# Kernel optimization log

Measured on AMD Instinct MI355X. Metric: run time of the kernel, lower is better.

## Reference

```python
import jax, jax.numpy as jnp
import numpy as np

EPS = 1e-5
# NOTE: TransmorpherLayer2d passes (dim_head, num_heads) into TiedAxialSelfAttention2d(num_heads, dim_head),
# so with init dim_head=64, num_heads=8 the attention effectively uses H=64 heads of C=8 channels each.
H = 64
C = 8


def _ln_ch(x, w, b):
    # AxialLayerNorm over channel dim (dim=1) of [B, D, S, L]
    m = x.mean(axis=1, keepdims=True)
    v = x.var(axis=1, keepdims=True)
    return (x - m) * jax.lax.rsqrt(v + EPS) * w[None, :, None, None] + b[None, :, None, None]


def _conv1x1(x, W, b):
    # Conv2d kernel_size=1: pointwise channel mix. W: [out, in], x: [B, in, S, L]
    return jnp.einsum('od,bdsl->bosl', W, x) + b[None, :, None, None]


def setup_inputs() -> dict:
    key = jax.random.key(0)
    ks = jax.random.split(key, 8)
    B, D, S, L, F = 1, 512, 64, 256, 2048
    g = lambda k, shape: jax.random.normal(k, shape, jnp.float32) * 0.02
    return {
        'x': jax.random.normal(ks[0], (B, D, S, L), jnp.float32),
        'w_row': g(ks[1], (3 * D, D)), 'b_row': jnp.zeros((3 * D,), jnp.float32),
        'w_col': g(ks[2], (3 * D, D)), 'b_col': jnp.zeros((3 * D,), jnp.float32),
        'w_an1': jnp.ones((D,), jnp.float32), 'b_an1': jnp.zeros((D,), jnp.float32),
        'w_an2': jnp.ones((D,), jnp.float32), 'b_an2': jnp.zeros((D,), jnp.float32),
        'w_ff1': g(ks[3], (F, D)), 'b_ff1': jnp.zeros((F,), jnp.float32),
        'w_ff2': g(ks[4], (D, F)), 'b_ff2': jnp.zeros((D,), jnp.float32),
        'w_ln1': jnp.ones((D,), jnp.float32), 'b_ln1': jnp.zeros((D,), jnp.float32),
        'w_ln2': jnp.ones((D,), jnp.float32), 'b_ln2': jnp.zeros((D,), jnp.float32),
    }


def _forward(x, w_row, b_row, w_col, b_col, w_an1, b_an1, w_an2, b_an2,
             w_ff1, b_ff1, w_ff2, b_ff2, w_ln1, b_ln1, w_ln2, b_ln2):
    B, D, S, L = x.shape
    # ---- tied row attention (attention tied across the S axis; no 1/sqrt scaling in source) ----
    qkv = _conv1x1(x, w_row, b_row)
    q, k, v = [t.reshape(B, H, C, S, L) for t in jnp.split(qkv, 3, axis=1)]
    row_attn = jax.nn.softmax(jnp.einsum('bhcsi,bhcsj->bhij', q, k), axis=-1)  # [B,H,L,L]
    row_out = jnp.einsum('bhij,bhdsj->bhdsi', row_attn, v).reshape(B, D, S, L)
    out = _ln_ch(x + row_out, w_an1, b_an1)
    # ---- column attention (softmax over key index j = dim -2) ----
    qkv = _conv1x1(out, w_col, b_col)
    q, k, v = [t.reshape(B, H, C, S, L) for t in jnp.split(qkv, 3, axis=1)]
    col_attn = jax.nn.softmax(jnp.einsum('bhcil,bhcjl->bhijl', q, k), axis=-2)  # [B,H,S,S,L]
    col_out = jnp.einsum('bhijl,bhdjl->bhdil', col_attn, v).reshape(B, D, S, L)
    attn_out = _ln_ch(out + col_out, w_an2, b_an2)
    # ---- layer body. Source bug kept faithfully: the attention residual `x + dropout1(out)`
    # is computed then discarded; norm1 is applied to the attention output only. ----
    h = _ln_ch(attn_out, w_ln1, b_ln1)
    ff = _conv1x1(jax.nn.relu(_conv1x1(h, w_ff1, b_ff1)), w_ff2, b_ff2)
    return _ln_ch(h + ff, w_ln2, b_ln2)


def reference(x, w_row, b_row, w_col, b_col, w_an1, b_an1, w_an2, b_an2,
              w_ff1, b_ff1, w_ff2, b_ff2, w_ln1, b_ln1, w_ln2, b_ln2):
    return _forward(x, w_row, b_row, w_col, b_col, w_an1, b_an1, w_an2, b_an2,
                    w_ff1, b_ff1, w_ff2, b_ff2, w_ln1, b_ln1, w_ln2, b_ln2)
```

## Files before the change

### kernel.cpp

```cpp
#include <hip/hip_runtime.h>
#include <hip/hip_bf16.h>

using s16x8 = __attribute__((ext_vector_type(8))) short;
using f32x4 = __attribute__((ext_vector_type(4))) float;
using u32x2 = __attribute__((ext_vector_type(2))) unsigned;

__device__ __forceinline__ ushort f2bf(float f) {
  union { float f; unsigned u; } v; v.f = f;
  unsigned r = v.u + 0x7fffu + ((v.u >> 16) & 1u);
  return (ushort)(r >> 16);
}
__device__ __forceinline__ float bf2f(ushort u) {
  return __uint_as_float(((unsigned)u) << 16);
}
__device__ __forceinline__ void gload16(const void* g, void* l) {
  __builtin_amdgcn_global_load_lds(
      (const __attribute__((address_space(1))) void*)g,
      (__attribute__((address_space(3))) void*)l, 16, 0, 0);
}

template<int AF, int BF, bool BIAS, bool RELU, int OUT, bool TRC>
__global__ __launch_bounds__(256)
void gemm(void* __restrict__ Cv, const ushort* __restrict__ A,
          const ushort* __restrict__ B, const float* __restrict__ bias,
          int K, int lda, int ldb, int ldc, long sA, long sB, long sC)
{
  __shared__ ushort As[2][5120];
  __shared__ ushort Bs[2][5120];
  const int tid  = threadIdx.x;
  const int lane = tid & 63, wid = tid >> 6;
  const int m0 = blockIdx.y * 128, n0 = blockIdx.x * 128;
  A += (long)blockIdx.z * sA;
  B += (long)blockIdx.z * sB;

  const int wm = (wid >> 1) * 64, wn = (wid & 1) * 64;
  const int fr = lane & 15, kg = lane >> 4;

  f32x4 acc[4][4];
#pragma unroll
  for (int i = 0; i < 4; ++i)
#pragma unroll
    for (int j = 0; j < 4; ++j)
#pragma unroll
      for (int r = 0; r < 4; ++r) acc[i][j][r] = 0.f;

  auto stageT = [&](const ushort* __restrict__ G, int ld, int c0,
                    ushort* lds, int k0) {
#pragma unroll
    for (int c = 0; c < 2; ++c) {
      const int nb = wid * 2 + c;
      const ushort* gp = G + (long)(k0 + (lane >> 1)) * ld + c0 + nb * 16 + (lane & 1) * 8;
      gload16(gp, lds + nb * 512);
    }
  };
  auto loadN = [&](const ushort* __restrict__ G, int ld, int r0, int k0,
                   uint4& x, uint4& y) {
    const ushort* gp = G + (long)(r0 + (tid >> 1)) * ld + k0 + (tid & 1) * 8;
    x = *(const uint4*)gp;
    y = *(const uint4*)(gp + 16);
  };
  auto writeN = [&](ushort* lds, uint4 x, uint4 y) {
    ushort* p = lds + (tid >> 1) * 40 + (tid & 1) * 8;
    *(uint4*)p = x;
    *(uint4*)(p + 16) = y;
  };
  auto fragN = [&](const ushort* lds, int row) {
    union { s16x8 f; u32x2 h[2]; } u;
    const ushort* p = lds + row * 40 + kg * 4;
    u.h[0] = *(const u32x2*)p;
    u.h[1] = *(const u32x2*)(p + 16);
    return u.f;
  };
  auto fragT = [&](const ushort* lds, int rb) {
    union { s16x8 f; u32x2 h[2]; } u;
    unsigned base = (unsigned)(unsigned long long)(lds + rb * 512) + lane * 8;
    asm volatile("ds_read_b64_tr_b16 %0, %1" : "=v"(u.h[0]) : "v"(base));
    asm volatile("ds_read_b64_tr_b16 %0, %1 offset:512" : "=v"(u.h[1]) : "v"(base));
    return u.f;
  };

  const int NT = K >> 5;
  uint4 ax, ay, bx, by;

  if constexpr (AF == 0) { loadN(A, lda, m0, 0, ax, ay); writeN(As[0], ax, ay); }
  else                   { stageT(A, lda, m0, As[0], 0); }
  if constexpr (BF == 0) { loadN(B, ldb, n0, 0, bx, by); writeN(Bs[0], bx, by); }
  else                   { stageT(B, ldb, n0, Bs[0], 0); }
  __syncthreads();

  for (int t = 0; t < NT; ++t) {
    const int cur = t & 1, nxt = cur ^ 1;
    const bool pre = (t + 1) < NT;
    if (pre) {
      if constexpr (AF == 0) loadN(A, lda, m0, (t + 1) << 5, ax, ay);
      else                   stageT(A, lda, m0, As[nxt], (t + 1) << 5);
      if constexpr (BF == 0) loadN(B, ldb, n0, (t + 1) << 5, bx, by);
      else                   stageT(B, ldb, n0, Bs[nxt], (t + 1) << 5);
    }
    s16x8 af[4], bv[4];
#pragma unroll
    for (int m = 0; m < 4; ++m) {
      if constexpr (AF == 0) af[m] = fragN(As[cur], wm + m * 16 + fr);
      else                   af[m] = fragT(As[cur], (wm >> 4) + m);
    }
#pragma unroll
    for (int n = 0; n < 4; ++n) {
      if constexpr (BF == 0) bv[n] = fragN(Bs[cur], wn + n * 16 + fr);
      else                   bv[n] = fragT(Bs[cur], (wn >> 4) + n);
    }
    if constexpr (AF == 1 || BF == 1) {
      asm volatile("s_waitcnt lgkmcnt(0)");
      __builtin_amdgcn_sched_barrier(0);
    }
    __builtin_amdgcn_s_setprio(1);
#pragma unroll
    for (int m = 0; m < 4; ++m)
#pragma unroll
      for (int n = 0; n < 4; ++n)
        acc[m][n] = __builtin_amdgcn_mfma_f32_16x16x32_bf16(af[m], bv[n], acc[m][n], 0, 0, 0);
    __builtin_amdgcn_s_setprio(0);
    if (pre) {
      if constexpr (AF == 0) writeN(As[nxt], ax, ay);
      if constexpr (BF == 0) writeN(Bs[nxt], bx, by);
    }
    __syncthreads();
  }

#pragma unroll
  for (int m = 0; m < 4; ++m) {
    const int rowb = m0 + wm + m * 16 + kg * 4;
#pragma unroll
    for (int n = 0; n < 4; ++n) {
      const int col = n0 + wn + n * 16 + fr;
      f32x4 v = acc[m][n];
      if constexpr (BIAS) {
#pragma unroll
        for (int r = 0; r < 4; ++r) v[r] += bias[rowb + r];
      }
      if constexpr (RELU) {
#pragma unroll
        for (int r = 0; r < 4; ++r) v[r] = fmaxf(v[r], 0.f);
      }
      if constexpr (TRC) {
        float* C = (float*)Cv + (long)blockIdx.z * sC;
        float4 s; s.x = v[0]; s.y = v[1]; s.z = v[2]; s.w = v[3];
        *(float4*)(C + (long)col * ldc + rowb) = s;
      } else if constexpr (OUT == 0) {
        float* C = (float*)Cv + (long)blockIdx.z * sC;
#pragma unroll
        for (int r = 0; r < 4; ++r) C[(long)(rowb + r) * ldc + col] = v[r];
      } else {
        ushort* C = (ushort*)Cv + (long)blockIdx.z * sC;
#pragma unroll
        for (int r = 0; r < 4; ++r) C[(long)(rowb + r) * ldc + col] = f2bf(v[r]);
      }
    }
  }
}

__global__ __launch_bounds__(256)
void cvt_kernel(const float4* __restrict__ in, ushort4* __restrict__ out, int n4) {
  int i = blockIdx.x * 256 + threadIdx.x;
  if (i < n4) {
    float4 f = in[i];
    ushort4 u; u.x = f2bf(f.x); u.y = f2bf(f.y); u.z = f2bf(f.z); u.w = f2bf(f.w);
    out[i] = u;
  }
}

__global__ __launch_bounds__(256)
void softmax_kernel(const float* __restrict__ S, ushort* __restrict__ P) {
  const int row = blockIdx.x * 4 + (threadIdx.x >> 6);
  const int lane = threadIdx.x & 63;
  float4 v = *(const float4*)(S + (long)row * 256 + lane * 4);
  float mx = fmaxf(fmaxf(v.x, v.y), fmaxf(v.z, v.w));
#pragma unroll
  for (int off = 32; off; off >>= 1) mx = fmaxf(mx, __shfl_xor(mx, off));
  v.x = __expf(v.x - mx); v.y = __expf(v.y - mx);
  v.z = __expf(v.z - mx); v.w = __expf(v.w - mx);
  float s = v.x + v.y + v.z + v.w;
#pragma unroll
  for (int off = 32; off; off >>= 1) s += __shfl_xor(s, off);
  const float r = 1.f / s;
  ushort4 o;
  o.x = f2bf(v.x * r); o.y = f2bf(v.y * r); o.z = f2bf(v.z * r); o.w = f2bf(v.w * r);
  *(ushort4*)(P + (long)row * 256 + lane * 4) = o;
}

__global__ __launch_bounds__(256)
void colattn_kernel(const ushort* __restrict__ qkv, float* __restrict__ out) {
  __shared__ float q[4][8][64], kk[4][8][64], vv[4][8][64];
  const int h = blockIdx.y;
  const int l0 = blockIdx.x * 4;
  const int tid = threadIdx.x;
  for (int i = tid; i < 1536; i += 256) {
    int m = i >> 9;
    int e = i & 511;
    int c = e >> 6, s = e & 63;
    ushort4 u = *(const ushort4*)(qkv + (long)(m * 512 + h * 8 + c) * 16384 + s * 256 + l0);
    float* dst = (m == 0) ? &q[0][0][0] : (m == 1) ? &kk[0][0][0] : &vv[0][0][0];
    dst[e] = bf2f(u.x); dst[512 + e] = bf2f(u.y);
    dst[1024 + e] = bf2f(u.z); dst[1536 + e] = bf2f(u.w);
  }
  __syncthreads();
  const int li = tid >> 6, lane = tid & 63;
  float qi[8];
#pragma unroll
  for (int c = 0; c < 8; ++c) qi[c] = q[li][c][lane];
  float sc[64];
#pragma unroll
  for (int j = 0; j < 64; ++j) {
    float s = 0.f;
#pragma unroll
    for (int c = 0; c < 8; ++c) s += qi[c] * kk[li][c][j];
    sc[j] = s;
  }
  float mx = sc[0];
#pragma unroll
  for (int j = 1; j < 64; ++j) mx = fmaxf(mx, sc[j]);
  float sum = 0.f;
#pragma unroll
  for (int j = 0; j < 64; ++j) { sc[j] = __expf(sc[j] - mx); sum += sc[j]; }
  const float rs = 1.f / sum;
  float o[8];
#pragma unroll
  for (int c = 0; c < 8; ++c) o[c] = 0.f;
#pragma unroll
  for (int j = 0; j < 64; ++j)
#pragma unroll
    for (int c = 0; c < 8; ++c) o[c] += sc[j] * vv[li][c][j];
#pragma unroll
  for (int c = 0; c < 8; ++c) q[li][c][lane] = o[c] * rs;
  __syncthreads();
  for (int i = tid; i < 512; i += 256) {
    int c = i >> 6, s = i & 63;
    float4 f; f.x = q[0][c][s]; f.y = q[1][c][s]; f.z = q[2][c][s]; f.w = q[3][c][s];
    *(float4*)(out + (long)(h * 8 + c) * 16384 + s * 256 + l0) = f;
  }
}

template<bool RES, bool BFO>
__global__ __launch_bounds__(256)
void ln_kernel(float* __restrict__ out, ushort* __restrict__ bfo,
               const float* __restrict__ a, const float* __restrict__ b,
               const float* __restrict__ w, const float* __restrict__ bias) {
  __shared__ float red[8][64];
  const int lane = threadIdx.x & 63;
  const int seg = threadIdx.x >> 6;
  const long n = (long)blockIdx.x * 64 + lane;
  float s1 = 0.f, s2 = 0.f;
  for (int d = seg * 128; d < seg * 128 + 128; ++d) {
    float v = a[(long)d * 16384 + n];
    if constexpr (RES) v += b[(long)d * 16384 + n];
    s1 += v; s2 += v * v;
  }
  red[seg][lane] = s1; red[4 + seg][lane] = s2;
  __syncthreads();
  s1 = red[0][lane] + red[1][lane] + red[2][lane] + red[3][lane];
  s2 = red[4][lane] + red[5][lane] + red[6][lane] + red[7][lane];
  const float mean = s1 * (1.f / 512.f);
  const float var = s2 * (1.f / 512.f) - mean * mean;
  const float rstd = rsqrtf(var + 1e-5f);
  for (int d = seg * 128; d < seg * 128 + 128; ++d) {
    float v = a[(long)d * 16384 + n];
    if constexpr (RES) v += b[(long)d * 16384 + n];
    float o = (v - mean) * rstd * w[d] + bias[d];
    out[(long)d * 16384 + n] = o;
    if constexpr (BFO) bfo[(long)d * 16384 + n] = f2bf(o);
  }
}

extern "C" void kernel_launch(void* const* d_in, const int* in_sizes, int n_in,
                              void* d_out, int out_size, void* d_ws, size_t ws_size,
                              hipStream_t stream) {
  const float* x     = (const float*)d_in[0];
  const float* w_row = (const float*)d_in[1];
  const float* b_row = (const float*)d_in[2];
  const float* w_col = (const float*)d_in[3];
  const float* b_col = (const float*)d_in[4];
  const float* w_an1 = (const float*)d_in[5];
  const float* b_an1 = (const float*)d_in[6];
  const float* w_an2 = (const float*)d_in[7];
  const float* b_an2 = (const float*)d_in[8];
  const float* w_ff1 = (const float*)d_in[9];
  const float* b_ff1 = (const float*)d_in[10];
  const float* w_ff2 = (const float*)d_in[11];
  const float* b_ff2 = (const float*)d_in[12];
  const float* w_ln1 = (const float*)d_in[13];
  const float* b_ln1 = (const float*)d_in[14];
  const float* w_ln2 = (const float*)d_in[15];
  const float* b_ln2 = (const float*)d_in[16];
  float* outp = (float*)d_out;

  char* Wb = (char*)d_ws;
  ushort* big   = (ushort*)Wb;
  float*  sc    = (float*)(Wb + (size_t)1536 * 16384 * 2);
  float*  bufA  = (float*)(Wb + 67108864ull);
  float*  bufB  = (float*)(Wb + 100663296ull);
  float*  bufC  = (float*)(Wb + 134217728ull);
  ushort* P     = (ushort*)bufC;
  ushort* actbf = (ushort*)(Wb + 167772160ull);
  ushort* xbf   = actbf;
  ushort* wrowb = (ushort*)(Wb + 184549376ull);
  ushort* wcolb = wrowb + 786432;
  ushort* wff1b = wcolb + 786432;
  ushort* wff2b = wff1b + 1048576;

  const dim3 blk(256);
  const long HQ = 131072;
  const long HS = 65536;

  cvt_kernel<<<8192, blk, 0, stream>>>((const float4*)x, (ushort4*)xbf, 2097152);
  cvt_kernel<<<768,  blk, 0, stream>>>((const float4*)w_row, (ushort4*)wrowb, 196608);
  cvt_kernel<<<768,  blk, 0, stream>>>((const float4*)w_col, (ushort4*)wcolb, 196608);
  cvt_kernel<<<1024, blk, 0, stream>>>((const float4*)w_ff1, (ushort4*)wff1b, 262144);
  cvt_kernel<<<1024, blk, 0, stream>>>((const float4*)w_ff2, (ushort4*)wff2b, 262144);

  gemm<0,1,true,false,1,false><<<dim3(128, 12, 1), blk, 0, stream>>>(
      big, wrowb, xbf, b_row, 512, 512, 16384, 16384, 0, 0, 0);
  gemm<1,1,false,false,0,false><<<dim3(2, 2, 64), blk, 0, stream>>>(
      sc, big, big + (long)512 * 16384, nullptr, 512, 256, 256, 256, HQ, HQ, HS);
  softmax_kernel<<<4096, blk, 0, stream>>>(sc, P);
  gemm<0,0,false,false,0,true><<<dim3(4, 2, 64), blk, 0, stream>>>(
      bufA, P, big + (long)1024 * 16384, nullptr, 256, 256, 256, 256, HS, HQ, HQ);
  ln_kernel<true, true><<<256, blk, 0, stream>>>(bufB, actbf, x, bufA, w_an1, b_an1);
  gemm<0,1,true,false,1,false><<<dim3(128, 12, 1), blk, 0, stream>>>(
      big, wcolb, actbf, b_col, 512, 512, 16384, 16384, 0, 0, 0);
  colattn_kernel<<<dim3(64, 64), blk, 0, stream>>>(big, bufA);
  ln_kernel<true, false><<<256, blk, 0, stream>>>(bufC, nullptr, bufB, bufA, w_an2, b_an2);
  ln_kernel<false, true><<<256, blk, 0, stream>>>(bufB, actbf, bufC, nullptr, w_ln1, b_ln1);
  gemm<0,1,true,true,1,false><<<dim3(128, 16, 1), blk, 0, stream>>>(
      big, wff1b, actbf, b_ff1, 512, 512, 16384, 16384, 0, 0, 0);
  gemm<0,1,true,false,0,false><<<dim3(128, 4, 1), blk, 0, stream>>>(
      bufA, wff2b, big, b_ff2, 2048, 2048, 16384, 16384, 0, 0, 0);
  ln_kernel<true, false><<<256, blk, 0, stream>>>(outp, nullptr, bufB, bufA, w_ln2, b_ln2);
}
```

Baseline: 531.1 us.

## Swizzle block order for XCD locality, fuse back-to-back layernorms, cache LN values in registers

GEMM and column-attention blocks are remapped so that consecutive workgroups, which round-robin across XCDs, cover contiguous tiles, aiming at better L2 reuse. Layernorm kernels now use 1024 threads and keep each element in registers, so the input is read once instead of twice. The two consecutive layernorms after column attention are fused into one kernel with two reductions, dropping an intermediate fp32 buffer round trip. The fused kernel reads from and writes to bufB in place, which is safe only because every element is held in registers before any write.

```diff
diff --git a/kernel.cpp b/kernel.cpp
--- a/kernel.cpp
+++ b/kernel.cpp
@@ -29,7 +29,10 @@
   __shared__ ushort Bs[2][5120];
   const int tid  = threadIdx.x;
   const int lane = tid & 63, wid = tid >> 6;
-  const int m0 = blockIdx.y * 128, n0 = blockIdx.x * 128;
+  const int nwg = gridDim.x * gridDim.y;
+  const int lin = blockIdx.y * gridDim.x + blockIdx.x;
+  const int swz = ((nwg & 7) == 0) ? ((lin & 7) * (nwg >> 3) + (lin >> 3)) : lin;
+  const int m0 = (swz / gridDim.x) * 128, n0 = (swz % gridDim.x) * 128;
   A += (long)blockIdx.z * sA;
   B += (long)blockIdx.z * sB;
 
@@ -190,8 +193,10 @@
 __global__ __launch_bounds__(256)
 void colattn_kernel(const ushort* __restrict__ qkv, float* __restrict__ out) {
   __shared__ float q[4][8][64], kk[4][8][64], vv[4][8][64];
-  const int h = blockIdx.y;
-  const int l0 = blockIdx.x * 4;
+  const int lin = blockIdx.x;
+  const int swz = (lin & 7) * 512 + (lin >> 3);
+  const int h = swz >> 6;
+  const int l0 = (swz & 63) * 4;
   const int tid = threadIdx.x;
   for (int i = tid; i < 1536; i += 256) {
     int m = i >> 9;
@@ -240,33 +245,82 @@
 }
 
 template<bool RES, bool BFO>
-__global__ __launch_bounds__(256)
+__global__ __launch_bounds__(1024)
 void ln_kernel(float* __restrict__ out, ushort* __restrict__ bfo,
                const float* __restrict__ a, const float* __restrict__ b,
                const float* __restrict__ w, const float* __restrict__ bias) {
-  __shared__ float red[8][64];
-  const int lane = threadIdx.x & 63;
-  const int seg = threadIdx.x >> 6;
+  __shared__ float red[2][16][64];
+  const int lane = threadIdx.x & 63, seg = threadIdx.x >> 6;
   const long n = (long)blockIdx.x * 64 + lane;
+  const int d0 = seg * 32;
+  float v[32];
   float s1 = 0.f, s2 = 0.f;
-  for (int d = seg * 128; d < seg * 128 + 128; ++d) {
-    float v = a[(long)d * 16384 + n];
-    if constexpr (RES) v += b[(long)d * 16384 + n];
-    s1 += v; s2 += v * v;
-  }
-  red[seg][lane] = s1; red[4 + seg][lane] = s2;
-  __syncthreads();
-  s1 = red[0][lane] + red[1][lane] + red[2][lane] + red[3][lane];
-  s2 = red[4][lane] + red[5][lane] + red[6][lane] + red[7][lane];
+#pragma unroll
+  for (int i = 0; i < 32; ++i) {
+    float t = a[(long)(d0 + i) * 16384 + n];
+    if constexpr (RES) t += b[(long)(d0 + i) * 16384 + n];
+    v[i] = t; s1 += t; s2 += t * t;
+  }
+  red[0][seg][lane] = s1; red[1][seg][lane] = s2;
+  __syncthreads();
+  s1 = 0.f; s2 = 0.f;
+#pragma unroll
+  for (int s = 0; s < 16; ++s) { s1 += red[0][s][lane]; s2 += red[1][s][lane]; }
   const float mean = s1 * (1.f / 512.f);
   const float var = s2 * (1.f / 512.f) - mean * mean;
   const float rstd = rsqrtf(var + 1e-5f);
-  for (int d = seg * 128; d < seg * 128 + 128; ++d) {
-    float v = a[(long)d * 16384 + n];
-    if constexpr (RES) v += b[(long)d * 16384 + n];
-    float o = (v - mean) * rstd * w[d] + bias[d];
-    out[(long)d * 16384 + n] = o;
-    if constexpr (BFO) bfo[(long)d * 16384 + n] = f2bf(o);
+#pragma unroll
+  for (int i = 0; i < 32; ++i) {
+    float o = (v[i] - mean) * rstd * w[d0 + i] + bias[d0 + i];
+    out[(long)(d0 + i) * 16384 + n] = o;
+    if constexpr (BFO) bfo[(long)(d0 + i) * 16384 + n] = f2bf(o);
+  }
+}
+
+__global__ __launch_bounds__(1024)
+void ln_fuse_kernel(float* __restrict__ out, ushort* __restrict__ bfo,
+                    const float* __restrict__ a, const float* __restrict__ b,
+                    const float* __restrict__ w1, const float* __restrict__ b1,
+                    const float* __restrict__ w2, const float* __restrict__ b2) {
+  __shared__ float red[2][16][64];
+  const int lane = threadIdx.x & 63, seg = threadIdx.x >> 6;
+  const long n = (long)blockIdx.x * 64 + lane;
+  const int d0 = seg * 32;
+  float v[32];
+  float s1 = 0.f, s2 = 0.f;
+#pragma unroll
+  for (int i = 0; i < 32; ++i) {
+    float t = a[(long)(d0 + i) * 16384 + n] + b[(long)(d0 + i) * 16384 + n];
+    v[i] = t; s1 += t; s2 += t * t;
+  }
+  red[0][seg][lane] = s1; red[1][seg][lane] = s2;
+  __syncthreads();
+  s1 = 0.f; s2 = 0.f;
+#pragma unroll
+  for (int s = 0; s < 16; ++s) { s1 += red[0][s][lane]; s2 += red[1][s][lane]; }
+  float mean = s1 * (1.f / 512.f);
+  float var = s2 * (1.f / 512.f) - mean * mean;
+  float rstd = rsqrtf(var + 1e-5f);
+  __syncthreads();
+  s1 = 0.f; s2 = 0.f;
+#pragma unroll
+  for (int i = 0; i < 32; ++i) {
+    float y = (v[i] - mean) * rstd * w1[d0 + i] + b1[d0 + i];
+    v[i] = y; s1 += y; s2 += y * y;
+  }
+  red[0][seg][lane] = s1; red[1][seg][lane] = s2;
+  __syncthreads();
+  s1 = 0.f; s2 = 0.f;
+#pragma unroll
+  for (int s = 0; s < 16; ++s) { s1 += red[0][s][lane]; s2 += red[1][s][lane]; }
+  mean = s1 * (1.f / 512.f);
+  var = s2 * (1.f / 512.f) - mean * mean;
+  rstd = rsqrtf(var + 1e-5f);
+#pragma unroll
+  for (int i = 0; i < 32; ++i) {
+    float o = (v[i] - mean) * rstd * w2[d0 + i] + b2[d0 + i];
+    out[(long)(d0 + i) * 16384 + n] = o;
+    bfo[(long)(d0 + i) * 16384 + n] = f2bf(o);
   }
 }
 
@@ -297,8 +351,7 @@
   float*  sc    = (float*)(Wb + (size_t)1536 * 16384 * 2);
   float*  bufA  = (float*)(Wb + 67108864ull);
   float*  bufB  = (float*)(Wb + 100663296ull);
-  float*  bufC  = (float*)(Wb + 134217728ull);
-  ushort* P     = (ushort*)bufC;
+  ushort* P     = (ushort*)(Wb + 134217728ull);
   ushort* actbf = (ushort*)(Wb + 167772160ull);
   ushort* xbf   = actbf;
   ushort* wrowb = (ushort*)(Wb + 184549376ull);
@@ -323,15 +376,15 @@
   softmax_kernel<<<4096, blk, 0, stream>>>(sc, P);
   gemm<0,0,false,false,0,true><<<dim3(4, 2, 64), blk, 0, stream>>>(
       bufA, P, big + (long)1024 * 16384, nullptr, 256, 256, 256, 256, HS, HQ, HQ);
-  ln_kernel<true, true><<<256, blk, 0, stream>>>(bufB, actbf, x, bufA, w_an1, b_an1);
+  ln_kernel<true, true><<<256, dim3(1024), 0, stream>>>(bufB, actbf, x, bufA, w_an1, b_an1);
   gemm<0,1,true,false,1,false><<<dim3(128, 12, 1), blk, 0, stream>>>(
       big, wcolb, actbf, b_col, 512, 512, 16384, 16384, 0, 0, 0);
-  colattn_kernel<<<dim3(64, 64), blk, 0, stream>>>(big, bufA);
-  ln_kernel<true, false><<<256, blk, 0, stream>>>(bufC, nullptr, bufB, bufA, w_an2, b_an2);
-  ln_kernel<false, true><<<256, blk, 0, stream>>>(bufB, actbf, bufC, nullptr, w_ln1, b_ln1);
+  colattn_kernel<<<4096, blk, 0, stream>>>(big, bufA);
+  ln_fuse_kernel<<<256, dim3(1024), 0, stream>>>(bufB, actbf, bufB, bufA,
+                                                 w_an2, b_an2, w_ln1, b_ln1);
   gemm<0,1,true,true,1,false><<<dim3(128, 16, 1), blk, 0, stream>>>(
       big, wff1b, actbf, b_ff1, 512, 512, 16384, 16384, 0, 0, 0);
   gemm<0,1,true,false,0,false><<<dim3(128, 4, 1), blk, 0, stream>>>(
       bufA, wff2b, big, b_ff2, 2048, 2048, 16384, 16384, 0, 0, 0);
-  ln_kernel<true, false><<<256, blk, 0, stream>>>(outp, nullptr, bufB, bufA, w_ln2, b_ln2);
-}
+  ln_kernel<true, false><<<256, dim3(1024), 0, stream>>>(outp, nullptr, bufB, bufA, w_ln2, b_ln2);
+}
```

New measurement: 499.1 us. -6.0%, faster.
